# Optimization experiments

Hardware: AMD Instinct MI355X
Metric: run time of the kernel (lower is better)

The kernel has to match this reference:

```python
import jax, jax.numpy as jnp
import numpy as np
import math

B, T, H = 32, 2048, 512  # batch, seq, hidden (= input_size)

def setup_inputs() -> dict:
    key = jax.random.key(0)
    ks = jax.random.split(key, 13)
    stdv = 1.0 / math.sqrt(H)
    def u(k, shape):
        return jax.random.uniform(k, shape, jnp.float32, -stdv, stdv)
    inp = {"x": jax.random.normal(ks[0], (B, T, H), jnp.float32)}
    names = ["U_i", "V_i", "b_i", "U_f", "V_f", "b_f", "U_c", "V_c", "b_c", "U_o", "V_o", "b_o"]
    for i, n in enumerate(names):
        shape = (H,) if n.startswith("b") else (H, H)
        inp[n] = u(ks[i + 1], shape)
    return inp

def reference(x, U_i, V_i, b_i, U_f, V_f, b_f, U_c, V_c, b_c, U_o, V_o, b_o):
    batch = x.shape[0]
    hidden = U_i.shape[1]
    # Precompute input projections for all timesteps (same math, hoisted out of the loop)
    U = jnp.stack([U_i, U_f, U_c, U_o], axis=0)        # [4, H, H]
    V = jnp.stack([V_i, V_f, V_c, V_o], axis=0)        # [4, H, H]
    b = jnp.stack([b_i, b_f, b_c, b_o], axis=0)        # [4, H]
    xU = jnp.einsum("bti,gih->tbgh", x, U) + b          # [T, B, 4, H]

    h0 = jnp.zeros((batch, hidden), x.dtype)
    c0 = jnp.zeros((batch, hidden), x.dtype)

    def step(carry, xu_t):
        h, c = carry
        gates = xu_t + jnp.einsum("bh,ghk->bgk", h, V)  # [B, 4, H]
        i_t = jax.nn.sigmoid(gates[:, 0])
        f_t = jax.nn.sigmoid(gates[:, 1])
        g_t = jnp.tanh(gates[:, 2])
        o_t = jax.nn.sigmoid(gates[:, 3])
        c_new = f_t * c + i_t * g_t
        h_new = o_t * jnp.tanh(c_new)
        return (h_new, c_new), h_new

    (h_T, c_T), hs = jax.lax.scan(step, (h0, c0), xU)   # hs: [T, B, H]
    hidden_seq = jnp.transpose(hs, (1, 0, 2))           # [B, T, H]
    return hidden_seq, (h_T, c_T)
```

## Files before the change

kernel.cpp:

```cpp
#include <hip/hip_runtime.h>


#define BB 32
#define TT 2048
#define HH 512
#define NWG 32
#define HS (BB*TT*HH)

typedef short short8 __attribute__((ext_vector_type(8)));
typedef float floatx4 __attribute__((ext_vector_type(4)));

__device__ __forceinline__ unsigned short f2bf(float f) {
  union { float f; unsigned u; } v; v.f = f;
  return (unsigned short)((v.u + 0x7FFFu + ((v.u >> 16) & 1u)) >> 16);
}
__device__ __forceinline__ unsigned pk2(float a, float b) {
  return (unsigned)f2bf(a) | ((unsigned)f2bf(b) << 16);
}
__device__ __forceinline__ float sigm(float z) { return 1.0f / (1.0f + __expf(-z)); }
__device__ __forceinline__ float tanh_fast(float z) { return 1.0f - 2.0f / (__expf(2.0f * z) + 1.0f); }

#define LOADF(IDX) __hip_atomic_load(&flags[(IDX)], __ATOMIC_RELAXED, __HIP_MEMORY_SCOPE_AGENT)

#define LOAD_X(XR, HALFBASE, TSTEP)                                              \
    if (tid >= 128) {                                                            \
      _Pragma("unroll")                                                          \
      for (int rr = 0; rr < 6; ++rr) {                                           \
        const int i = rr * 384 + sx;                                             \
        if (i < 2048) {                                                          \
          const int grow = (HALFBASE) + (i >> 7), c4 = i & 127;                  \
          XR[rr] = *(const float4*)(x + ((size_t)grow * TT + (TSTEP)) * HH + c4 * 4); \
        }                                                                        \
      }                                                                          \
    }

#define STAGE_X(XR, HALFBASE)                                                    \
    if (tid >= 128) {                                                            \
      _Pragma("unroll")                                                          \
      for (int rr = 0; rr < 6; ++rr) {                                           \
        const int i = rr * 384 + sx;                                             \
        if (i < 2048) {                                                          \
          const int grow = (HALFBASE) + (i >> 7), c4 = i & 127;                  \
          uint2 p; p.x = pk2(XR[rr].x, XR[rr].y); p.y = pk2(XR[rr].z, XR[rr].w); \
          *(uint2*)(lds_x + ((grow * 1024 + c4 * 8) ^ ((grow & 7) << 4))) = p;   \
        }                                                                        \
      }                                                                          \
    }

#define EW_PHASE(HALF, C0, C1, SLOTPTR)                                          \
    if (tid < 128) {                                                             \
      const int er = tid >> 3, ec = (tid & 7) * 2;                               \
      float zz[4][2];                                                            \
      _Pragma("unroll")                                                          \
      for (int g = 0; g < 4; ++g) {                                              \
        zz[g][0] = gates[0][g][er][ec]     + gates[1][g][er][ec]     + bia[g][0];\
        zz[g][1] = gates[0][g][er][ec + 1] + gates[1][g][er][ec + 1] + bia[g][1];\
      }                                                                          \
      const float i0 = sigm(zz[0][0]), i1 = sigm(zz[0][1]);                      \
      const float f0 = sigm(zz[1][0]), f1 = sigm(zz[1][1]);                      \
      const float g0 = tanh_fast(zz[2][0]), g1 = tanh_fast(zz[2][1]);            \
      const float o0 = sigm(zz[3][0]), o1 = sigm(zz[3][1]);                      \
      C0 = f0 * C0 + i0 * g0;  C1 = f1 * C1 + i1 * g1;                           \
      const float h0 = o0 * tanh_fast(C0), h1 = o1 * tanh_fast(C1);              \
      const int gc = j0 + ec;                                                    \
      *(float2*)(out + ((size_t)((HALF)*16 + er) * TT + t) * HH + gc) =          \
          make_float2(h0, h1);                                                   \
      const int uidx = (((gc >> 5) * 64 + ((gc >> 3) & 3) * 16 + er) * 4) + ((gc & 7) >> 1); \
      __hip_atomic_store((unsigned*)(SLOTPTR) + uidx, pk2(h0, h1),               \
                         __ATOMIC_RELAXED, __HIP_MEMORY_SCOPE_AGENT);            \
      if (t == TT - 1) {                                                         \
        const int b = (HALF)*16 + er;                                            \
        out[(size_t)HS + b * HH + gc]               = h0;                        \
        out[(size_t)HS + b * HH + gc + 1]           = h1;                        \
        out[(size_t)HS + BB * HH + b * HH + gc]     = C0;                        \
        out[(size_t)HS + BB * HH + b * HH + gc + 1] = C1;                        \
      }                                                                          \
    }

__global__ __launch_bounds__(512, 1)
void lstm_kernel(const float* __restrict__ x,
                 const float* __restrict__ Ui, const float* __restrict__ Vi, const float* __restrict__ bi,
                 const float* __restrict__ Uf, const float* __restrict__ Vf, const float* __restrict__ bf,
                 const float* __restrict__ Uc, const float* __restrict__ Vc, const float* __restrict__ bc,
                 const float* __restrict__ Uo, const float* __restrict__ Vo, const float* __restrict__ bo,
                 float* __restrict__ out,
                 unsigned long long* __restrict__ hbuf,
                 unsigned* __restrict__ flags)
{
  __shared__ __align__(16) unsigned char lds_x[BB * HH * 2];
  __shared__ __align__(16) float gates[2][4][16][18];

  const int tid  = threadIdx.x;
  const int wg   = blockIdx.x;
  const int lane = tid & 63;
  const int wid  = tid >> 6;
  const int sub  = wid & 1;
  const int gt   = wid >> 1;
  const int j0   = wg * 16;
  const int ln   = lane & 15;
  const int hi   = lane >> 4;
  const int sx   = tid - 128;

  const int xsw    = (ln & 7) << 4;
  const int xbaseP = ln * 1024 + hi * 16;
  const int xbaseQ = (16 + ln) * 1024 + hi * 16;
  const int hfb    = sub * 1024 + lane * 2;

  const float* Ug = (gt == 0) ? Ui : (gt == 1) ? Uf : (gt == 2) ? Uc : Uo;
  const float* Vg = (gt == 0) ? Vi : (gt == 1) ? Vf : (gt == 2) ? Vc : Vo;

  short8 ufr[8], vfr[8];
#pragma unroll
  for (int kcl = 0; kcl < 8; ++kcl) {
    const int kc = sub * 8 + kcl;
    short8 a, b;
#pragma unroll
    for (int i = 0; i < 8; ++i) {
      const int krow = kc * 32 + hi * 8 + i;
      a[i] = (short)f2bf(Ug[(size_t)krow * HH + j0 + ln]);
      b[i] = (short)f2bf(Vg[(size_t)krow * HH + j0 + ln]);
    }
    ufr[kcl] = a; vfr[kcl] = b;
  }

  float bia[4][2];
  float cP0 = 0.f, cP1 = 0.f, cQ0 = 0.f, cQ1 = 0.f;
  if (tid < 128) {
    const int ec = (tid & 7) * 2;
    bia[0][0] = bi[j0 + ec]; bia[0][1] = bi[j0 + ec + 1];
    bia[1][0] = bf[j0 + ec]; bia[1][1] = bf[j0 + ec + 1];
    bia[2][0] = bc[j0 + ec]; bia[2][1] = bc[j0 + ec + 1];
    bia[3][0] = bo[j0 + ec]; bia[3][1] = bo[j0 + ec + 1];
  }

#pragma unroll
  for (int rr = 0; rr < 8; ++rr) {
    const int i = rr * 512 + tid;
    const int grow = i >> 7, c4 = i & 127;
    const float4 v = *(const float4*)(x + (size_t)grow * TT * HH + c4 * 4);
    uint2 p; p.x = pk2(v.x, v.y); p.y = pk2(v.z, v.w);
    *(uint2*)(lds_x + ((grow * 1024 + c4 * 8) ^ ((grow & 7) << 4))) = p;
  }
  float4 xa[6], xb[6];
  LOAD_X(xa, 0, 1)
  __syncthreads();

  union HU { unsigned long long q[2]; short8 s; };
  HU hreg[8];
  unsigned fP = 0, fQ = 0;

  for (int t = 0; t < TT; ++t) {
    const int par = t & 1;
    if (t > 0) fQ = LOADF(32 + (lane & 31));
    if (t + 1 < TT) LOAD_X(xb, 16, t + 1)

    floatx4 acc = {0.f, 0.f, 0.f, 0.f};
#pragma unroll
    for (int kcl = 0; kcl < 8; ++kcl) {
      const short8 xf = *(const short8*)(lds_x + ((xbaseP + (sub * 8 + kcl) * 64) ^ xsw));
      acc = __builtin_amdgcn_mfma_f32_16x16x32_bf16(xf, ufr[kcl], acc, 0, 0, 0);
    }
    if (t > 0) {
#pragma unroll
      for (int kcl = 0; kcl < 8; ++kcl)
        acc = __builtin_amdgcn_mfma_f32_16x16x32_bf16(hreg[kcl].s, vfr[kcl], acc, 0, 0, 0);
    }
#pragma unroll
    for (int rg = 0; rg < 4; ++rg) gates[sub][gt][hi * 4 + rg][ln] = acc[rg];
    __syncthreads();

    if (t > 0) {
      const unsigned tq = (unsigned)t;
      while (!__all((int)(fQ >= tq))) {
        __builtin_amdgcn_s_sleep(1);
        fQ = LOADF(32 + (lane & 31));
      }
      const unsigned long long* hq = hbuf + (size_t)(2 + ((t - 1) & 1)) * 2048;
#pragma unroll
      for (int kcl = 0; kcl < 8; ++kcl) {
        hreg[kcl].q[0] = __hip_atomic_load(hq + hfb + kcl * 128,     __ATOMIC_RELAXED, __HIP_MEMORY_SCOPE_AGENT);
        hreg[kcl].q[1] = __hip_atomic_load(hq + hfb + kcl * 128 + 1, __ATOMIC_RELAXED, __HIP_MEMORY_SCOPE_AGENT);
      }
    }

    EW_PHASE(0, cP0, cP1, hbuf + (size_t)par * 2048)
    if (t + 1 < TT) STAGE_X(xa, 0)
    __syncthreads();
    if (tid == 0)
      __hip_atomic_store(&flags[wg], (unsigned)(t + 1), __ATOMIC_RELAXED, __HIP_MEMORY_SCOPE_AGENT);

    acc = (floatx4){0.f, 0.f, 0.f, 0.f};
#pragma unroll
    for (int kcl = 0; kcl < 8; ++kcl) {
      const short8 xf = *(const short8*)(lds_x + ((xbaseQ + (sub * 8 + kcl) * 64) ^ xsw));
      acc = __builtin_amdgcn_mfma_f32_16x16x32_bf16(xf, ufr[kcl], acc, 0, 0, 0);
    }
    if (t > 0) {
#pragma unroll
      for (int kcl = 0; kcl < 8; ++kcl)
        acc = __builtin_amdgcn_mfma_f32_16x16x32_bf16(hreg[kcl].s, vfr[kcl], acc, 0, 0, 0);
    }
    if (t + 1 < TT) fP = LOADF(lane & 31);
#pragma unroll
    for (int rg = 0; rg < 4; ++rg) gates[sub][gt][hi * 4 + rg][ln] = acc[rg];
    __syncthreads();

    EW_PHASE(1, cQ0, cQ1, hbuf + (size_t)(2 + par) * 2048)
    if (t + 1 < TT) STAGE_X(xb, 16)
    __syncthreads();
    if (tid == 0)
      __hip_atomic_store(&flags[32 + wg], (unsigned)(t + 1), __ATOMIC_RELAXED, __HIP_MEMORY_SCOPE_AGENT);

    if (t + 1 < TT) {
      const unsigned tp = (unsigned)(t + 1);
      while (!__all((int)(fP >= tp))) {
        __builtin_amdgcn_s_sleep(1);
        fP = LOADF(lane & 31);
      }
      const unsigned long long* hp = hbuf + (size_t)par * 2048;
#pragma unroll
      for (int kcl = 0; kcl < 8; ++kcl) {
        hreg[kcl].q[0] = __hip_atomic_load(hp + hfb + kcl * 128,     __ATOMIC_RELAXED, __HIP_MEMORY_SCOPE_AGENT);
        hreg[kcl].q[1] = __hip_atomic_load(hp + hfb + kcl * 128 + 1, __ATOMIC_RELAXED, __HIP_MEMORY_SCOPE_AGENT);
      }
      if (t + 2 < TT) LOAD_X(xa, 0, t + 2)
    }
  }
}

extern "C" void kernel_launch(void* const* d_in, const int* in_sizes, int n_in,
                              void* d_out, int out_size, void* d_ws, size_t ws_size,
                              hipStream_t stream) {
  (void)in_sizes; (void)n_in; (void)out_size; (void)ws_size;
  const float* x  = (const float*)d_in[0];
  const float* Ui = (const float*)d_in[1];
  const float* Vi = (const float*)d_in[2];
  const float* bi = (const float*)d_in[3];
  const float* Uf = (const float*)d_in[4];
  const float* Vf = (const float*)d_in[5];
  const float* bf = (const float*)d_in[6];
  const float* Uc = (const float*)d_in[7];
  const float* Vc = (const float*)d_in[8];
  const float* bc = (const float*)d_in[9];
  const float* Uo = (const float*)d_in[10];
  const float* Vo = (const float*)d_in[11];
  const float* bo = (const float*)d_in[12];

  unsigned long long* hbuf = (unsigned long long*)d_ws;
  unsigned* flags = (unsigned*)((char*)d_ws + 65536);

  hipMemsetAsync((char*)d_ws + 65536, 0, 256, stream);

  lstm_kernel<<<dim3(NWG), dim3(512), 0, stream>>>(
      x, Ui, Vi, bi, Uf, Vf, bf, Uc, Vc, bc, Uo, Vo, bo,
      (float*)d_out, hbuf, flags);
}
```

Measured before the change: 10.72 ms.

## Replace flag-based inter-workgroup sync with tagged h values and hoist x-projection MFMAs

Result: slower. 39.71 ms (+270.4%).

```diff
diff --git a/kernel.cpp b/kernel.cpp
--- a/kernel.cpp
+++ b/kernel.cpp
@@ -10,71 +10,129 @@
 typedef short short8 __attribute__((ext_vector_type(8)));
 typedef float floatx4 __attribute__((ext_vector_type(4)));
 
-__device__ __forceinline__ unsigned short f2bf(float f) {
+static __device__ __forceinline__ unsigned short f2bf(float f) {
   union { float f; unsigned u; } v; v.f = f;
   return (unsigned short)((v.u + 0x7FFFu + ((v.u >> 16) & 1u)) >> 16);
 }
-__device__ __forceinline__ unsigned pk2(float a, float b) {
+static __device__ __forceinline__ unsigned pk2(float a, float b) {
   return (unsigned)f2bf(a) | ((unsigned)f2bf(b) << 16);
 }
-__device__ __forceinline__ float sigm(float z) { return 1.0f / (1.0f + __expf(-z)); }
-__device__ __forceinline__ float tanh_fast(float z) { return 1.0f - 2.0f / (__expf(2.0f * z) + 1.0f); }
-
-#define LOADF(IDX) __hip_atomic_load(&flags[(IDX)], __ATOMIC_RELAXED, __HIP_MEMORY_SCOPE_AGENT)
-
-#define LOAD_X(XR, HALFBASE, TSTEP)                                              \
-    if (tid >= 128) {                                                            \
-      _Pragma("unroll")                                                          \
-      for (int rr = 0; rr < 6; ++rr) {                                           \
-        const int i = rr * 384 + sx;                                             \
-        if (i < 2048) {                                                          \
-          const int grow = (HALFBASE) + (i >> 7), c4 = i & 127;                  \
-          XR[rr] = *(const float4*)(x + ((size_t)grow * TT + (TSTEP)) * HH + c4 * 4); \
-        }                                                                        \
-      }                                                                          \
-    }
-
-#define STAGE_X(XR, HALFBASE)                                                    \
-    if (tid >= 128) {                                                            \
-      _Pragma("unroll")                                                          \
-      for (int rr = 0; rr < 6; ++rr) {                                           \
-        const int i = rr * 384 + sx;                                             \
-        if (i < 2048) {                                                          \
-          const int grow = (HALFBASE) + (i >> 7), c4 = i & 127;                  \
-          uint2 p; p.x = pk2(XR[rr].x, XR[rr].y); p.y = pk2(XR[rr].z, XR[rr].w); \
-          *(uint2*)(lds_x + ((grow * 1024 + c4 * 8) ^ ((grow & 7) << 4))) = p;   \
-        }                                                                        \
-      }                                                                          \
-    }
-
-#define EW_PHASE(HALF, C0, C1, SLOTPTR)                                          \
-    if (tid < 128) {                                                             \
-      const int er = tid >> 3, ec = (tid & 7) * 2;                               \
-      float zz[4][2];                                                            \
-      _Pragma("unroll")                                                          \
-      for (int g = 0; g < 4; ++g) {                                              \
-        zz[g][0] = gates[0][g][er][ec]     + gates[1][g][er][ec]     + bia[g][0];\
-        zz[g][1] = gates[0][g][er][ec + 1] + gates[1][g][er][ec + 1] + bia[g][1];\
-      }                                                                          \
-      const float i0 = sigm(zz[0][0]), i1 = sigm(zz[0][1]);                      \
-      const float f0 = sigm(zz[1][0]), f1 = sigm(zz[1][1]);                      \
-      const float g0 = tanh_fast(zz[2][0]), g1 = tanh_fast(zz[2][1]);            \
-      const float o0 = sigm(zz[3][0]), o1 = sigm(zz[3][1]);                      \
-      C0 = f0 * C0 + i0 * g0;  C1 = f1 * C1 + i1 * g1;                           \
-      const float h0 = o0 * tanh_fast(C0), h1 = o1 * tanh_fast(C1);              \
-      const int gc = j0 + ec;                                                    \
-      *(float2*)(out + ((size_t)((HALF)*16 + er) * TT + t) * HH + gc) =          \
-          make_float2(h0, h1);                                                   \
-      const int uidx = (((gc >> 5) * 64 + ((gc >> 3) & 3) * 16 + er) * 4) + ((gc & 7) >> 1); \
-      __hip_atomic_store((unsigned*)(SLOTPTR) + uidx, pk2(h0, h1),               \
-                         __ATOMIC_RELAXED, __HIP_MEMORY_SCOPE_AGENT);            \
-      if (t == TT - 1) {                                                         \
-        const int b = (HALF)*16 + er;                                            \
-        out[(size_t)HS + b * HH + gc]               = h0;                        \
-        out[(size_t)HS + b * HH + gc + 1]           = h1;                        \
-        out[(size_t)HS + BB * HH + b * HH + gc]     = C0;                        \
-        out[(size_t)HS + BB * HH + b * HH + gc + 1] = C1;                        \
-      }                                                                          \
+static __device__ __forceinline__ float sigm(float z) { return 1.f / (1.f + __expf(-z)); }
+static __device__ __forceinline__ float tanh_fast(float z) { return 1.f - 2.f / (__expf(2.f * z) + 1.f); }
+
+static __device__ __forceinline__ unsigned long long aldq(const void* p) {
+  return __hip_atomic_load((const unsigned long long*)p, __ATOMIC_RELAXED, __HIP_MEMORY_SCOPE_AGENT);
+}
+static __device__ __forceinline__ void astq(void* p, unsigned long long v) {
+  __hip_atomic_store((unsigned long long*)p, v, __ATOMIC_RELAXED, __HIP_MEMORY_SCOPE_AGENT);
+}
+static __device__ __forceinline__ void lgkm0() {
+  asm volatile("s_waitcnt lgkmcnt(0)" ::: "memory");
+  __builtin_amdgcn_sched_barrier(0);
+}
+static __device__ __forceinline__ void rawbar() {
+  __builtin_amdgcn_sched_barrier(0);
+  __builtin_amdgcn_s_barrier();
+  __builtin_amdgcn_sched_barrier(0);
+}
+static __device__ __forceinline__ unsigned tagOf(int t) {
+  return 1u + ((unsigned)(t >> 1) % 3u);
+}
+
+
+#define LOAD_X(XR, HALFBASE, TS)                                                  \
+    if (tid >= 128) {                                                             \
+      _Pragma("unroll")                                                           \
+      for (int rr = 0; rr < 6; ++rr) {                                            \
+        const int i = rr * 384 + sx;                                              \
+        if (i < 2048) {                                                           \
+          const int grow = (HALFBASE) + (i >> 7), c4 = i & 127;                   \
+          XR[rr] = *(const float4*)(x + ((size_t)grow * TT + (TS)) * HH + c4 * 4);\
+        }                                                                         \
+      }                                                                           \
+    }
+
+#define STAGE_X(XR, HALFBASE)                                                     \
+    if (tid >= 128) {                                                             \
+      _Pragma("unroll")                                                           \
+      for (int rr = 0; rr < 6; ++rr) {                                            \
+        const int i = rr * 384 + sx;                                              \
+        if (i < 2048) {                                                           \
+          const int grow = (HALFBASE) + (i >> 7), c4 = i & 127;                   \
+          uint2 p; p.x = pk2(XR[rr].x, XR[rr].y); p.y = pk2(XR[rr].z, XR[rr].w);  \
+          *(uint2*)(lds_x + ((grow * 1024 + c4 * 8) ^ ((grow & 7) << 4))) = p;    \
+        }                                                                         \
+      }                                                                           \
+    }
+
+#define POLL_H(SLOTOFF, TG)                                                       \
+    {                                                                             \
+      const unsigned char* sl_ = ws + (SLOTOFF);                                  \
+      const int cb_ = ln * 2048 + sub * 1024 + hi * 32;                           \
+      unsigned long long rw_[8][4];                                               \
+      _Pragma("unroll")                                                           \
+      for (int kc_ = 0; kc_ < 8; ++kc_)                                           \
+        { _Pragma("unroll")                                                       \
+          for (int j_ = 0; j_ < 4; ++j_)                                          \
+            rw_[kc_][j_] = aldq(sl_ + cb_ + kc_ * 128 + j_ * 8); }                \
+      _Pragma("unroll")                                                           \
+      for (int kc_ = 0; kc_ < 8; ++kc_) {                                         \
+        int it_ = 0;                                                              \
+        for (;;) {                                                                \
+          bool ok_ = true;                                                        \
+          _Pragma("unroll")                                                       \
+          for (int j_ = 0; j_ < 4; ++j_) {                                        \
+            const unsigned long long q_ = rw_[kc_][j_];                           \
+            ok_ = ok_ && ((unsigned)(q_ & 3u) == (TG))                            \
+                      && ((unsigned)((q_ >> 32) & 3u) == (TG));                   \
+          }                                                                       \
+          if (__all((int)ok_)) break;                                             \
+          if (++it_ > (1 << 17)) break;                                           \
+          __builtin_amdgcn_s_sleep(1);                                            \
+          _Pragma("unroll")                                                       \
+          for (int j_ = 0; j_ < 4; ++j_)                                          \
+            rw_[kc_][j_] = aldq(sl_ + cb_ + kc_ * 128 + j_ * 8);                  \
+        }                                                                         \
+        short8 fr_;                                                               \
+        _Pragma("unroll")                                                         \
+        for (int j_ = 0; j_ < 4; ++j_) {                                          \
+          union { unsigned long long q; float f[2]; } u_; u_.q = rw_[kc_][j_];    \
+          fr_[2 * j_]     = (short)f2bf(u_.f[0]);                                 \
+          fr_[2 * j_ + 1] = (short)f2bf(u_.f[1]);                                 \
+        }                                                                         \
+        hreg[kc_] = fr_;                                                          \
+      }                                                                           \
+    }
+
+#define EW_DO(ROWBASE, CREF, SLOTOFF, TG)                                         \
+    if (tid < 128) {                                                              \
+      float z0_[4], z1_[4];                                                       \
+      _Pragma("unroll")                                                           \
+      for (int g_ = 0; g_ < 4; ++g_) {                                            \
+        z0_[g_] = gates[0][g_][er][ec2]     + gates[1][g_][er][ec2]     + bia[g_][0]; \
+        z1_[g_] = gates[0][g_][er][ec2 + 1] + gates[1][g_][er][ec2 + 1] + bia[g_][1]; \
+      }                                                                           \
+      const float i0_ = sigm(z0_[0]), i1_ = sigm(z1_[0]);                         \
+      const float f0_ = sigm(z0_[1]), f1_ = sigm(z1_[1]);                         \
+      const float g0_ = tanh_fast(z0_[2]), g1_ = tanh_fast(z1_[2]);               \
+      const float o0_ = sigm(z0_[3]), o1_ = sigm(z1_[3]);                         \
+      CREF##0 = f0_ * CREF##0 + i0_ * g0_;                                        \
+      CREF##1 = f1_ * CREF##1 + i1_ * g1_;                                        \
+      const float h0_ = o0_ * tanh_fast(CREF##0);                                 \
+      const float h1_ = o1_ * tanh_fast(CREF##1);                                 \
+      const unsigned u0_ = (__float_as_uint(h0_) & ~3u) | (TG);                   \
+      const unsigned u1_ = (__float_as_uint(h1_) & ~3u) | (TG);                   \
+      astq(ws + (SLOTOFF) + er * 2048 + (j0 + ec2) * 4,                           \
+           (unsigned long long)u0_ | ((unsigned long long)u1_ << 32));            \
+      *(float2*)(out + ((size_t)((ROWBASE) + er) * TT + t) * HH + j0 + ec2) =     \
+          make_float2(h0_, h1_);                                                  \
+      if (t == TT - 1) {                                                          \
+        const int b_ = (ROWBASE) + er;                                            \
+        out[(size_t)HS + b_ * HH + j0 + ec2]               = h0_;                 \
+        out[(size_t)HS + b_ * HH + j0 + ec2 + 1]           = h1_;                 \
+        out[(size_t)HS + BB * HH + b_ * HH + j0 + ec2]     = CREF##0;             \
+        out[(size_t)HS + BB * HH + b_ * HH + j0 + ec2 + 1] = CREF##1;             \
+      }                                                                           \
     }
 
 __global__ __launch_bounds__(512, 1)
@@ -83,12 +141,10 @@
                  const float* __restrict__ Uf, const float* __restrict__ Vf, const float* __restrict__ bf,
                  const float* __restrict__ Uc, const float* __restrict__ Vc, const float* __restrict__ bc,
                  const float* __restrict__ Uo, const float* __restrict__ Vo, const float* __restrict__ bo,
-                 float* __restrict__ out,
-                 unsigned long long* __restrict__ hbuf,
-                 unsigned* __restrict__ flags)
+                 float* __restrict__ out, unsigned char* __restrict__ ws)
 {
   __shared__ __align__(16) unsigned char lds_x[BB * HH * 2];
-  __shared__ __align__(16) float gates[2][4][16][18];
+  __shared__ __align__(16) float gates[2][4][16][17];
 
   const int tid  = threadIdx.x;
   const int wg   = blockIdx.x;
@@ -100,11 +156,7 @@
   const int ln   = lane & 15;
   const int hi   = lane >> 4;
   const int sx   = tid - 128;
-
-  const int xsw    = (ln & 7) << 4;
-  const int xbaseP = ln * 1024 + hi * 16;
-  const int xbaseQ = (16 + ln) * 1024 + hi * 16;
-  const int hfb    = sub * 1024 + lane * 2;
+  const int xsw  = (ln & 7) << 4;
 
   const float* Ug = (gt == 0) ? Ui : (gt == 1) ? Uf : (gt == 2) ? Uc : Uo;
   const float* Vg = (gt == 0) ? Vi : (gt == 1) ? Vf : (gt == 2) ? Vc : Vo;
@@ -112,25 +164,25 @@
   short8 ufr[8], vfr[8];
 #pragma unroll
   for (int kcl = 0; kcl < 8; ++kcl) {
-    const int kc = sub * 8 + kcl;
     short8 a, b;
 #pragma unroll
     for (int i = 0; i < 8; ++i) {
-      const int krow = kc * 32 + hi * 8 + i;
+      const int krow = (sub * 8 + kcl) * 32 + hi * 8 + i;
       a[i] = (short)f2bf(Ug[(size_t)krow * HH + j0 + ln]);
       b[i] = (short)f2bf(Vg[(size_t)krow * HH + j0 + ln]);
     }
     ufr[kcl] = a; vfr[kcl] = b;
   }
 
+  const int er  = tid >> 3;
+  const int ec2 = (tid & 7) * 2;
   float bia[4][2];
   float cP0 = 0.f, cP1 = 0.f, cQ0 = 0.f, cQ1 = 0.f;
   if (tid < 128) {
-    const int ec = (tid & 7) * 2;
-    bia[0][0] = bi[j0 + ec]; bia[0][1] = bi[j0 + ec + 1];
-    bia[1][0] = bf[j0 + ec]; bia[1][1] = bf[j0 + ec + 1];
-    bia[2][0] = bc[j0 + ec]; bia[2][1] = bc[j0 + ec + 1];
-    bia[3][0] = bo[j0 + ec]; bia[3][1] = bo[j0 + ec + 1];
+    bia[0][0] = bi[j0 + ec2]; bia[0][1] = bi[j0 + ec2 + 1];
+    bia[1][0] = bf[j0 + ec2]; bia[1][1] = bf[j0 + ec2 + 1];
+    bia[2][0] = bc[j0 + ec2]; bia[2][1] = bc[j0 + ec2 + 1];
+    bia[3][0] = bo[j0 + ec2]; bia[3][1] = bo[j0 + ec2 + 1];
   }
 
 #pragma unroll
@@ -141,89 +193,91 @@
     uint2 p; p.x = pk2(v.x, v.y); p.y = pk2(v.z, v.w);
     *(uint2*)(lds_x + ((grow * 1024 + c4 * 8) ^ ((grow & 7) << 4))) = p;
   }
+  lgkm0();
+  rawbar();
+
+  floatx4 accU_P = {0.f, 0.f, 0.f, 0.f}, accU_Q = {0.f, 0.f, 0.f, 0.f};
+#pragma unroll
+  for (int kcl = 0; kcl < 8; ++kcl) {
+    const int kc = sub * 8 + kcl;
+    const short8 xf = *(const short8*)(lds_x + ((ln * 1024 + kc * 64 + hi * 16) ^ xsw));
+    accU_P = __builtin_amdgcn_mfma_f32_16x16x32_bf16(xf, ufr[kcl], accU_P, 0, 0, 0);
+  }
+#pragma unroll
+  for (int kcl = 0; kcl < 8; ++kcl) {
+    const int kc = sub * 8 + kcl;
+    const short8 xf = *(const short8*)(lds_x + (((16 + ln) * 1024 + kc * 64 + hi * 16) ^ xsw));
+    accU_Q = __builtin_amdgcn_mfma_f32_16x16x32_bf16(xf, ufr[kcl], accU_Q, 0, 0, 0);
+  }
+
   float4 xa[6], xb[6];
   LOAD_X(xa, 0, 1)
-  __syncthreads();
-
-  union HU { unsigned long long q[2]; short8 s; };
-  HU hreg[8];
-  unsigned fP = 0, fQ = 0;
+  LOAD_X(xb, 16, 1)
+
+  short8 hreg[8];
+#pragma unroll
+  for (int kcl = 0; kcl < 8; ++kcl) hreg[kcl] = short8{0,0,0,0,0,0,0,0};
 
   for (int t = 0; t < TT; ++t) {
-    const int par = t & 1;
-    if (t > 0) fQ = LOADF(32 + (lane & 31));
-    if (t + 1 < TT) LOAD_X(xb, 16, t + 1)
-
-    floatx4 acc = {0.f, 0.f, 0.f, 0.f};
-#pragma unroll
-    for (int kcl = 0; kcl < 8; ++kcl) {
-      const short8 xf = *(const short8*)(lds_x + ((xbaseP + (sub * 8 + kcl) * 64) ^ xsw));
-      acc = __builtin_amdgcn_mfma_f32_16x16x32_bf16(xf, ufr[kcl], acc, 0, 0, 0);
-    }
-    if (t > 0) {
-#pragma unroll
-      for (int kcl = 0; kcl < 8; ++kcl)
-        acc = __builtin_amdgcn_mfma_f32_16x16x32_bf16(hreg[kcl].s, vfr[kcl], acc, 0, 0, 0);
-    }
-#pragma unroll
-    for (int rg = 0; rg < 4; ++rg) gates[sub][gt][hi * 4 + rg][ln] = acc[rg];
-    __syncthreads();
-
-    if (t > 0) {
-      const unsigned tq = (unsigned)t;
-      while (!__all((int)(fQ >= tq))) {
-        __builtin_amdgcn_s_sleep(1);
-        fQ = LOADF(32 + (lane & 31));
+    const unsigned tg  = tagOf(t);
+    const int slotP = (t & 1) * 32768;
+    const int slotQ = 65536 + (t & 1) * 32768;
+
+    {
+      floatx4 a_ = accU_P;
+      if (t > 0) {
+#pragma unroll
+        for (int kcl = 0; kcl < 8; ++kcl)
+          a_ = __builtin_amdgcn_mfma_f32_16x16x32_bf16(hreg[kcl], vfr[kcl], a_, 0, 0, 0);
       }
-      const unsigned long long* hq = hbuf + (size_t)(2 + ((t - 1) & 1)) * 2048;
+#pragma unroll
+      for (int r = 0; r < 4; ++r) gates[sub][gt][hi * 4 + r][ln] = a_[r];
+    }
+    lgkm0();
+    rawbar();
+
+    EW_DO(0, cP, slotP, tg)
+    STAGE_X(xa, 0)
+    if (t > 0) POLL_H(65536 + ((t - 1) & 1) * 32768, tagOf(t - 1))
+    if (t + 2 < TT) LOAD_X(xa, 0, t + 2)
+    lgkm0();
+    rawbar();
+
+    {
+      floatx4 a_ = accU_Q;
+      if (t > 0) {
+#pragma unroll
+        for (int kcl = 0; kcl < 8; ++kcl)
+          a_ = __builtin_amdgcn_mfma_f32_16x16x32_bf16(hreg[kcl], vfr[kcl], a_, 0, 0, 0);
+      }
+#pragma unroll
+      for (int r = 0; r < 4; ++r) gates[sub][gt][hi * 4 + r][ln] = a_[r];
+    }
+    lgkm0();
+    rawbar();
+
+    EW_DO(16, cQ, slotQ, tg)
+    STAGE_X(xb, 16)
+    if (t + 1 < TT) POLL_H((t & 1) * 32768, tg)
+    if (t + 2 < TT) LOAD_X(xb, 16, t + 2)
+    lgkm0();
+    rawbar();
+
+    if (t + 1 < TT) {
+      floatx4 aP = {0.f, 0.f, 0.f, 0.f}, aQ = {0.f, 0.f, 0.f, 0.f};
 #pragma unroll
       for (int kcl = 0; kcl < 8; ++kcl) {
-        hreg[kcl].q[0] = __hip_atomic_load(hq + hfb + kcl * 128,     __ATOMIC_RELAXED, __HIP_MEMORY_SCOPE_AGENT);
-        hreg[kcl].q[1] = __hip_atomic_load(hq + hfb + kcl * 128 + 1, __ATOMIC_RELAXED, __HIP_MEMORY_SCOPE_AGENT);
+        const int kc = sub * 8 + kcl;
+        const short8 xf = *(const short8*)(lds_x + ((ln * 1024 + kc * 64 + hi * 16) ^ xsw));
+        aP = __builtin_amdgcn_mfma_f32_16x16x32_bf16(xf, ufr[kcl], aP, 0, 0, 0);
       }
-    }
-
-    EW_PHASE(0, cP0, cP1, hbuf + (size_t)par * 2048)
-    if (t + 1 < TT) STAGE_X(xa, 0)
-    __syncthreads();
-    if (tid == 0)
-      __hip_atomic_store(&flags[wg], (unsigned)(t + 1), __ATOMIC_RELAXED, __HIP_MEMORY_SCOPE_AGENT);
-
-    acc = (floatx4){0.f, 0.f, 0.f, 0.f};
-#pragma unroll
-    for (int kcl = 0; kcl < 8; ++kcl) {
-      const short8 xf = *(const short8*)(lds_x + ((xbaseQ + (sub * 8 + kcl) * 64) ^ xsw));
-      acc = __builtin_amdgcn_mfma_f32_16x16x32_bf16(xf, ufr[kcl], acc, 0, 0, 0);
-    }
-    if (t > 0) {
-#pragma unroll
-      for (int kcl = 0; kcl < 8; ++kcl)
-        acc = __builtin_amdgcn_mfma_f32_16x16x32_bf16(hreg[kcl].s, vfr[kcl], acc, 0, 0, 0);
-    }
-    if (t + 1 < TT) fP = LOADF(lane & 31);
-#pragma unroll
-    for (int rg = 0; rg < 4; ++rg) gates[sub][gt][hi * 4 + rg][ln] = acc[rg];
-    __syncthreads();
-
-    EW_PHASE(1, cQ0, cQ1, hbuf + (size_t)(2 + par) * 2048)
-    if (t + 1 < TT) STAGE_X(xb, 16)
-    __syncthreads();
-    if (tid == 0)
-      __hip_atomic_store(&flags[32 + wg], (unsigned)(t + 1), __ATOMIC_RELAXED, __HIP_MEMORY_SCOPE_AGENT);
-
-    if (t + 1 < TT) {
-      const unsigned tp = (unsigned)(t + 1);
-      while (!__all((int)(fP >= tp))) {
-        __builtin_amdgcn_s_sleep(1);
-        fP = LOADF(lane & 31);
+#pragma unroll
+      for (int kcl = 0; kcl < 8; ++kcl) {
+        const int kc = sub * 8 + kcl;
+        const short8 xf = *(const short8*)(lds_x + (((16 + ln) * 1024 + kc * 64 + hi * 16) ^ xsw));
+        aQ = __builtin_amdgcn_mfma_f32_16x16x32_bf16(xf, ufr[kcl], aQ, 0, 0, 0);
       }
-      const unsigned long long* hp = hbuf + (size_t)par * 2048;
-#pragma unroll
-      for (int kcl = 0; kcl < 8; ++kcl) {
-        hreg[kcl].q[0] = __hip_atomic_load(hp + hfb + kcl * 128,     __ATOMIC_RELAXED, __HIP_MEMORY_SCOPE_AGENT);
-        hreg[kcl].q[1] = __hip_atomic_load(hp + hfb + kcl * 128 + 1, __ATOMIC_RELAXED, __HIP_MEMORY_SCOPE_AGENT);
-      }
-      if (t + 2 < TT) LOAD_X(xa, 0, t + 2)
+      accU_P = aP; accU_Q = aQ;
     }
   }
 }
@@ -246,12 +300,9 @@
   const float* Vo = (const float*)d_in[11];
   const float* bo = (const float*)d_in[12];
 
-  unsigned long long* hbuf = (unsigned long long*)d_ws;
-  unsigned* flags = (unsigned*)((char*)d_ws + 65536);
-
-  hipMemsetAsync((char*)d_ws + 65536, 0, 256, stream);
+  hipMemsetAsync(d_ws, 0, 131072, stream);
 
   lstm_kernel<<<dim3(NWG), dim3(512), 0, stream>>>(
       x, Ui, Vi, bi, Uf, Vf, bf, Uc, Vc, bc, Uo, Vo, bo,
-      (float*)d_out, hbuf, flags);
-}
+      (float*)d_out, (unsigned char*)d_ws);
+}
```

## Co-locate persistent workgroups on one XCC and use L2-local sync loads

Applied to the files above, without the earlier changes.

Result: slower. 11.30 ms (+5.4%).

```diff
diff --git a/kernel.cpp b/kernel.cpp
--- a/kernel.cpp
+++ b/kernel.cpp
@@ -10,15 +10,40 @@
 typedef short short8 __attribute__((ext_vector_type(8)));
 typedef float floatx4 __attribute__((ext_vector_type(4)));
 
-__device__ __forceinline__ unsigned short f2bf(float f) {
+static __device__ __forceinline__ unsigned short f2bf(float f) {
   union { float f; unsigned u; } v; v.f = f;
   return (unsigned short)((v.u + 0x7FFFu + ((v.u >> 16) & 1u)) >> 16);
 }
-__device__ __forceinline__ unsigned pk2(float a, float b) {
+static __device__ __forceinline__ unsigned pk2(float a, float b) {
   return (unsigned)f2bf(a) | ((unsigned)f2bf(b) << 16);
 }
-__device__ __forceinline__ float sigm(float z) { return 1.0f / (1.0f + __expf(-z)); }
-__device__ __forceinline__ float tanh_fast(float z) { return 1.0f - 2.0f / (__expf(2.0f * z) + 1.0f); }
+static __device__ __forceinline__ float sigm(float z) { return 1.f / (1.f + __expf(-z)); }
+static __device__ __forceinline__ float tanh_fast(float z) { return 1.f - 2.f / (__expf(2.f * z) + 1.f); }
+
+static __device__ __forceinline__ unsigned long long aldq(const void* p) {
+  return __hip_atomic_load((const unsigned long long*)p, __ATOMIC_RELAXED, __HIP_MEMORY_SCOPE_AGENT);
+}
+static __device__ __forceinline__ unsigned agld(const unsigned* p) {
+  return __hip_atomic_load(p, __ATOMIC_RELAXED, __HIP_MEMORY_SCOPE_AGENT);
+}
+static __device__ __forceinline__ void ast4(unsigned* p, unsigned v) {
+  __hip_atomic_store(p, v, __ATOMIC_RELAXED, __HIP_MEMORY_SCOPE_AGENT);
+}
+static __device__ __forceinline__ unsigned ld_sc0dw(const void* p) {
+  unsigned r;
+  asm volatile("global_load_dword %0, %1, off sc0\n\ts_waitcnt vmcnt(0)"
+               : "=v"(r) : "v"(p) : "memory");
+  __builtin_amdgcn_sched_barrier(0);
+  return r;
+}
+static __device__ __forceinline__ void ld16_sc0_nw(int4& d, const void* p) {
+  asm volatile("global_load_dwordx4 %0, %1, off sc0" : "=v"(d) : "v"(p) : "memory");
+}
+static __device__ __forceinline__ void rawbar() {
+  __builtin_amdgcn_sched_barrier(0);
+  __builtin_amdgcn_s_barrier();
+  __builtin_amdgcn_sched_barrier(0);
+}
 
 #define LOADF(IDX) __hip_atomic_load(&flags[(IDX)], __ATOMIC_RELAXED, __HIP_MEMORY_SCOPE_AGENT)
 
@@ -66,8 +91,10 @@
       *(float2*)(out + ((size_t)((HALF)*16 + er) * TT + t) * HH + gc) =          \
           make_float2(h0, h1);                                                   \
       const int uidx = (((gc >> 5) * 64 + ((gc >> 3) & 3) * 16 + er) * 4) + ((gc & 7) >> 1); \
-      __hip_atomic_store((unsigned*)(SLOTPTR) + uidx, pk2(h0, h1),               \
-                         __ATOMIC_RELAXED, __HIP_MEMORY_SCOPE_AGENT);            \
+      unsigned* hw_ = (unsigned*)(SLOTPTR) + uidx;                               \
+      if (fastm) *(volatile unsigned*)hw_ = pk2(h0, h1);                         \
+      else __hip_atomic_store(hw_, pk2(h0, h1),                                  \
+                              __ATOMIC_RELAXED, __HIP_MEMORY_SCOPE_AGENT);       \
       if (t == TT - 1) {                                                         \
         const int b = (HALF)*16 + er;                                            \
         out[(size_t)HS + b * HH + gc]               = h0;                        \
@@ -83,15 +110,77 @@
                  const float* __restrict__ Uf, const float* __restrict__ Vf, const float* __restrict__ bf,
                  const float* __restrict__ Uc, const float* __restrict__ Vc, const float* __restrict__ bc,
                  const float* __restrict__ Uo, const float* __restrict__ Vo, const float* __restrict__ bo,
-                 float* __restrict__ out,
-                 unsigned long long* __restrict__ hbuf,
-                 unsigned* __restrict__ flags)
+                 float* __restrict__ out, unsigned char* __restrict__ ws)
 {
   __shared__ __align__(16) unsigned char lds_x[BB * HH * 2];
   __shared__ __align__(16) float gates[2][4][16][18];
-
-  const int tid  = threadIdx.x;
-  const int wg   = blockIdx.x;
+  __shared__ int s_rank, s_win, s_fast;
+
+  const int tid = threadIdx.x;
+  unsigned long long* hbuf = (unsigned long long*)ws;
+  unsigned* flags = (unsigned*)(ws + 65536);
+  unsigned* ectl  = (unsigned*)(ws + 66048);
+
+  int xcc;
+  asm volatile("s_getreg_b32 %0, hwreg(HW_REG_XCC_ID)" : "=s"(xcc));
+  xcc &= 7;
+  if (tid == 0) {
+    const int r = (int)atomicAdd(&ectl[xcc], 1u);
+    s_rank = r;
+    if (r == NWG - 1) atomicCAS(&ectl[8], 0u, (unsigned)(xcc + 1));
+  }
+  __syncthreads();
+  const int rank = s_rank;
+  __syncthreads();
+  if (tid == 0) {
+    unsigned w = 0; int it = 0;
+    while ((w = agld(&ectl[8])) == 0u && ++it < (1 << 20)) __builtin_amdgcn_s_sleep(8);
+    s_win = (int)w - 1;
+  }
+  __syncthreads();
+  const int win = s_win;
+  int wg;
+  bool member;
+  if (win >= 0) { member = (xcc == win) && (rank < NWG); wg = rank; }
+  else          { member = ((int)blockIdx.x < NWG);      wg = (int)blockIdx.x; }
+  if (!member) return;
+
+  int fastm = 0;
+  if (win >= 0) {
+    if (tid == 0) {
+      volatile unsigned* probe = (volatile unsigned*)(ws + 66560);
+      unsigned n1 = 0, n2 = 0; int it;
+      if (wg == 0) {
+        n1 = ((unsigned)__builtin_amdgcn_s_memrealtime() << 2) | 1u;
+        *probe = n1;
+        asm volatile("s_waitcnt vmcnt(0)" ::: "memory");
+        ast4(&ectl[11], n1);
+      }
+      it = 0; while ((n1 = agld(&ectl[11])) == 0u && ++it < (1 << 20)) __builtin_amdgcn_s_sleep(8);
+      int ok1 = 0;
+      for (it = 0; it < 4096 && !ok1; ++it)
+        if (ld_sc0dw((const void*)probe) == n1) ok1 = 1;
+      __hip_atomic_fetch_add(&ectl[13], 1u, __ATOMIC_RELAXED, __HIP_MEMORY_SCOPE_AGENT);
+      if (wg == 0) {
+        it = 0; while (agld(&ectl[13]) < (unsigned)NWG && ++it < (1 << 20)) __builtin_amdgcn_s_sleep(4);
+        n2 = n1 + 2u;
+        *probe = n2;
+        asm volatile("s_waitcnt vmcnt(0)" ::: "memory");
+        ast4(&ectl[12], n2);
+      }
+      it = 0; while ((n2 = agld(&ectl[12])) == 0u && ++it < (1 << 20)) __builtin_amdgcn_s_sleep(8);
+      int ok2 = 0;
+      for (it = 0; it < 256 && !ok2; ++it)
+        if (ld_sc0dw((const void*)probe) == n2) ok2 = 1;
+      if (ok1 && ok2) __hip_atomic_fetch_add(&ectl[9],  1u, __ATOMIC_RELAXED, __HIP_MEMORY_SCOPE_AGENT);
+      __hip_atomic_fetch_add(&ectl[10], 1u, __ATOMIC_RELAXED, __HIP_MEMORY_SCOPE_AGENT);
+      it = 0; while (agld(&ectl[10]) < (unsigned)NWG && ++it < (1 << 20)) __builtin_amdgcn_s_sleep(4);
+      s_fast = (agld(&ectl[9]) == (unsigned)NWG) ? 1 : 0;
+    }
+    __syncthreads();
+    fastm = s_fast;
+  }
+
   const int lane = tid & 63;
   const int wid  = tid >> 6;
   const int sub  = wid & 1;
@@ -100,11 +189,8 @@
   const int ln   = lane & 15;
   const int hi   = lane >> 4;
   const int sx   = tid - 128;
-
-  const int xsw    = (ln & 7) << 4;
-  const int xbaseP = ln * 1024 + hi * 16;
-  const int xbaseQ = (16 + ln) * 1024 + hi * 16;
-  const int hfb    = sub * 1024 + lane * 2;
+  const int xsw  = (ln & 7) << 4;
+  const int hfb  = sub * 1024 + lane * 2;
 
   const float* Ug = (gt == 0) ? Ui : (gt == 1) ? Uf : (gt == 2) ? Uc : Uo;
   const float* Vg = (gt == 0) ? Vi : (gt == 1) ? Vf : (gt == 2) ? Vc : Vo;
@@ -112,11 +198,10 @@
   short8 ufr[8], vfr[8];
 #pragma unroll
   for (int kcl = 0; kcl < 8; ++kcl) {
-    const int kc = sub * 8 + kcl;
     short8 a, b;
 #pragma unroll
     for (int i = 0; i < 8; ++i) {
-      const int krow = kc * 32 + hi * 8 + i;
+      const int krow = (sub * 8 + kcl) * 32 + hi * 8 + i;
       a[i] = (short)f2bf(Ug[(size_t)krow * HH + j0 + ln]);
       b[i] = (short)f2bf(Vg[(size_t)krow * HH + j0 + ln]);
     }
@@ -145,19 +230,20 @@
   LOAD_X(xa, 0, 1)
   __syncthreads();
 
-  union HU { unsigned long long q[2]; short8 s; };
+  union HU { unsigned long long q[2]; int4 v; short8 s; };
   HU hreg[8];
   unsigned fP = 0, fQ = 0;
 
   for (int t = 0; t < TT; ++t) {
     const int par = t & 1;
-    if (t > 0) fQ = LOADF(32 + (lane & 31));
+    if (t > 0 && !fastm) fQ = LOADF(32 + (lane & 31));
     if (t + 1 < TT) LOAD_X(xb, 16, t + 1)
 
     floatx4 acc = {0.f, 0.f, 0.f, 0.f};
 #pragma unroll
     for (int kcl = 0; kcl < 8; ++kcl) {
-      const short8 xf = *(const short8*)(lds_x + ((xbaseP + (sub * 8 + kcl) * 64) ^ xsw));
+      const int kc = sub * 8 + kcl;
+      const short8 xf = *(const short8*)(lds_x + ((ln * 1024 + kc * 64 + hi * 16) ^ xsw));
       acc = __builtin_amdgcn_mfma_f32_16x16x32_bf16(xf, ufr[kcl], acc, 0, 0, 0);
     }
     if (t > 0) {
@@ -170,29 +256,51 @@
     __syncthreads();
 
     if (t > 0) {
-      const unsigned tq = (unsigned)t;
-      while (!__all((int)(fQ >= tq))) {
-        __builtin_amdgcn_s_sleep(1);
-        fQ = LOADF(32 + (lane & 31));
-      }
-      const unsigned long long* hq = hbuf + (size_t)(2 + ((t - 1) & 1)) * 2048;
-#pragma unroll
-      for (int kcl = 0; kcl < 8; ++kcl) {
-        hreg[kcl].q[0] = __hip_atomic_load(hq + hfb + kcl * 128,     __ATOMIC_RELAXED, __HIP_MEMORY_SCOPE_AGENT);
-        hreg[kcl].q[1] = __hip_atomic_load(hq + hfb + kcl * 128 + 1, __ATOMIC_RELAXED, __HIP_MEMORY_SCOPE_AGENT);
+      if (fastm) {
+        if (tid < 128) {
+          const unsigned tq = (unsigned)t; int itc = 0;
+          for (;;) {
+            const unsigned v = ld_sc0dw(&flags[32 + (lane & 31)]);
+            if (__all((int)(v >= tq))) break;
+            if (++itc > (1 << 20)) break;
+            __builtin_amdgcn_s_sleep(1);
+          }
+        }
+        rawbar();
+        const unsigned char* hq =
+            (const unsigned char*)(hbuf + (size_t)(2 + ((t - 1) & 1)) * 2048);
+#pragma unroll
+        for (int kcl = 0; kcl < 8; ++kcl)
+          ld16_sc0_nw(hreg[kcl].v, hq + (size_t)(hfb + kcl * 128) * 8);
+      } else {
+        const unsigned tq = (unsigned)t; int itc = 0;
+        while (!__all((int)(fQ >= tq))) {
+          __builtin_amdgcn_s_sleep(1);
+          fQ = LOADF(32 + (lane & 31));
+          if (++itc > (1 << 20)) break;
+        }
+        const unsigned long long* hq = hbuf + (size_t)(2 + ((t - 1) & 1)) * 2048;
+#pragma unroll
+        for (int kcl = 0; kcl < 8; ++kcl) {
+          hreg[kcl].q[0] = aldq(hq + hfb + kcl * 128);
+          hreg[kcl].q[1] = aldq(hq + hfb + kcl * 128 + 1);
+        }
       }
     }
 
     EW_PHASE(0, cP0, cP1, hbuf + (size_t)par * 2048)
     if (t + 1 < TT) STAGE_X(xa, 0)
     __syncthreads();
-    if (tid == 0)
-      __hip_atomic_store(&flags[wg], (unsigned)(t + 1), __ATOMIC_RELAXED, __HIP_MEMORY_SCOPE_AGENT);
+    if (tid == 0 && t + 1 < TT) {
+      if (fastm) *(volatile unsigned*)&flags[wg] = (unsigned)(t + 1);
+      else       ast4(&flags[wg], (unsigned)(t + 1));
+    }
 
     acc = (floatx4){0.f, 0.f, 0.f, 0.f};
 #pragma unroll
     for (int kcl = 0; kcl < 8; ++kcl) {
-      const short8 xf = *(const short8*)(lds_x + ((xbaseQ + (sub * 8 + kcl) * 64) ^ xsw));
+      const int kc = sub * 8 + kcl;
+      const short8 xf = *(const short8*)(lds_x + (((16 + ln) * 1024 + kc * 64 + hi * 16) ^ xsw));
       acc = __builtin_amdgcn_mfma_f32_16x16x32_bf16(xf, ufr[kcl], acc, 0, 0, 0);
     }
     if (t > 0) {
@@ -200,7 +308,7 @@
       for (int kcl = 0; kcl < 8; ++kcl)
         acc = __builtin_amdgcn_mfma_f32_16x16x32_bf16(hreg[kcl].s, vfr[kcl], acc, 0, 0, 0);
     }
-    if (t + 1 < TT) fP = LOADF(lane & 31);
+    if (t + 1 < TT && !fastm) fP = LOADF(lane & 31);
 #pragma unroll
     for (int rg = 0; rg < 4; ++rg) gates[sub][gt][hi * 4 + rg][ln] = acc[rg];
     __syncthreads();
@@ -208,20 +316,40 @@
     EW_PHASE(1, cQ0, cQ1, hbuf + (size_t)(2 + par) * 2048)
     if (t + 1 < TT) STAGE_X(xb, 16)
     __syncthreads();
-    if (tid == 0)
-      __hip_atomic_store(&flags[32 + wg], (unsigned)(t + 1), __ATOMIC_RELAXED, __HIP_MEMORY_SCOPE_AGENT);
+    if (tid == 0 && t + 1 < TT) {
+      if (fastm) *(volatile unsigned*)&flags[32 + wg] = (unsigned)(t + 1);
+      else       ast4(&flags[32 + wg], (unsigned)(t + 1));
+    }
 
     if (t + 1 < TT) {
-      const unsigned tp = (unsigned)(t + 1);
-      while (!__all((int)(fP >= tp))) {
-        __builtin_amdgcn_s_sleep(1);
-        fP = LOADF(lane & 31);
-      }
-      const unsigned long long* hp = hbuf + (size_t)par * 2048;
-#pragma unroll
-      for (int kcl = 0; kcl < 8; ++kcl) {
-        hreg[kcl].q[0] = __hip_atomic_load(hp + hfb + kcl * 128,     __ATOMIC_RELAXED, __HIP_MEMORY_SCOPE_AGENT);
-        hreg[kcl].q[1] = __hip_atomic_load(hp + hfb + kcl * 128 + 1, __ATOMIC_RELAXED, __HIP_MEMORY_SCOPE_AGENT);
+      if (fastm) {
+        if (tid < 128) {
+          const unsigned tp = (unsigned)(t + 1); int itc = 0;
+          for (;;) {
+            const unsigned v = ld_sc0dw(&flags[lane & 31]);
+            if (__all((int)(v >= tp))) break;
+            if (++itc > (1 << 20)) break;
+            __builtin_amdgcn_s_sleep(1);
+          }
+        }
+        rawbar();
+        const unsigned char* hp = (const unsigned char*)(hbuf + (size_t)par * 2048);
+#pragma unroll
+        for (int kcl = 0; kcl < 8; ++kcl)
+          ld16_sc0_nw(hreg[kcl].v, hp + (size_t)(hfb + kcl * 128) * 8);
+      } else {
+        const unsigned tp = (unsigned)(t + 1); int itc = 0;
+        while (!__all((int)(fP >= tp))) {
+          __builtin_amdgcn_s_sleep(1);
+          fP = LOADF(lane & 31);
+          if (++itc > (1 << 20)) break;
+        }
+        const unsigned long long* hp = hbuf + (size_t)par * 2048;
+#pragma unroll
+        for (int kcl = 0; kcl < 8; ++kcl) {
+          hreg[kcl].q[0] = aldq(hp + hfb + kcl * 128);
+          hreg[kcl].q[1] = aldq(hp + hfb + kcl * 128 + 1);
+        }
       }
       if (t + 2 < TT) LOAD_X(xa, 0, t + 2)
     }
@@ -246,12 +374,9 @@
   const float* Vo = (const float*)d_in[11];
   const float* bo = (const float*)d_in[12];
 
-  unsigned long long* hbuf = (unsigned long long*)d_ws;
-  unsigned* flags = (unsigned*)((char*)d_ws + 65536);
-
-  hipMemsetAsync((char*)d_ws + 65536, 0, 256, stream);
-
-  lstm_kernel<<<dim3(NWG), dim3(512), 0, stream>>>(
+  hipMemsetAsync((char*)d_ws + 65536, 0, 4096, stream);
+
+  lstm_kernel<<<dim3(256), dim3(512), 0, stream>>>(
       x, Ui, Vi, bi, Uf, Vf, bf, Uc, Vc, bc, Uo, Vo, bo,
-      (float*)d_out, hbuf, flags);
-}
+      (float*)d_out, (unsigned char*)d_ws);
+}
```
